# Kernel optimization log

Hardware: AMD Instinct MI355X
Metric: run time of the kernel (lower is better)

## Reference

```python
import jax, jax.numpy as jnp
import numpy as np

B, S, D = 4, 4096, 2048
SCAN, STATE = 128, 16


def setup_inputs() -> dict:
    key = jax.random.key(0)
    ks = jax.random.split(key, 8)
    scale = 1.0 / np.sqrt(D)
    scale_s = 1.0 / np.sqrt(SCAN)
    x = jax.random.normal(ks[0], (B, S, D), dtype=jnp.float32)
    Wi = jax.random.normal(ks[1], (SCAN, D), dtype=jnp.float32) * scale
    Wo = jax.random.normal(ks[2], (D, SCAN), dtype=jnp.float32) * 0.02  # torch zero-inits; small random for nontrivial output
    A_log = jax.random.normal(ks[3], (SCAN, STATE), dtype=jnp.float32) * 0.1
    Wb = jax.random.normal(ks[4], (STATE, SCAN), dtype=jnp.float32) * scale_s
    Wc = jax.random.normal(ks[5], (STATE, SCAN), dtype=jnp.float32) * scale_s
    Wdt = jax.random.normal(ks[6], (SCAN, SCAN), dtype=jnp.float32) * scale_s
    b_dt = jnp.full((SCAN,), -3.0, dtype=jnp.float32)
    Wg = jax.random.normal(ks[7], (SCAN, D), dtype=jnp.float32) * scale
    return {"x": x, "Wi": Wi, "Wo": Wo, "A_log": A_log, "Wb": Wb,
            "Wc": Wc, "Wdt": Wdt, "b_dt": b_dt, "Wg": Wg}


def _selective_scan_ffn(x, Wi, Wo, A_log, Wb, Wc, Wdt, b_dt, Wg):
    z = jnp.einsum('bsd,nd->bsn', x, Wi)                      # [B,S,SCAN]
    gate = jax.nn.silu(jnp.einsum('bsd,nd->bsn', x, Wg))      # [B,S,SCAN]
    A = -jnp.exp(A_log)                                        # [SCAN,STATE]
    B_in = jnp.einsum('bsn,kn->bsk', z, Wb)                   # [B,S,STATE]
    C_in = jnp.einsum('bsn,kn->bsk', z, Wc)                   # [B,S,STATE]
    dt = jax.nn.softplus(jnp.einsum('bsn,mn->bsm', z, Wdt) + b_dt)  # [B,S,SCAN]
    A_bar = 1.0 + dt[..., None] * A                            # [B,S,SCAN,STATE]

    def step(state, inp):
        a_t, dt_t, z_t, b_t, c_t = inp
        # state: [B,SCAN,STATE]
        state = a_t * state + dt_t[..., None] * (z_t[..., None] * b_t[:, None, :])
        y = jnp.einsum('bnk,bk->bn', state, c_t)               # [B,SCAN]
        return state, y

    xs = (jnp.moveaxis(A_bar, 1, 0), jnp.moveaxis(dt, 1, 0),
          jnp.moveaxis(z, 1, 0), jnp.moveaxis(B_in, 1, 0), jnp.moveaxis(C_in, 1, 0))
    state0 = jnp.zeros((x.shape[0], Wi.shape[0], A_log.shape[1]), dtype=x.dtype)
    _, ys = jax.lax.scan(step, state0, xs)                     # [S,B,SCAN]
    y = jnp.moveaxis(ys, 0, 1) * gate                          # [B,S,SCAN]
    return jnp.einsum('bsn,dn->bsd', y, Wo)                    # [B,S,D]


def reference(x, Wi, Wo, A_log, Wb, Wc, Wdt, b_dt, Wg):
    return _selective_scan_ffn(x, Wi, Wo, A_log, Wb, Wc, Wdt, b_dt, Wg)
```

## Files before the change

### kernel.cpp

```cpp
#include <hip/hip_runtime.h>
#include <hip/hip_bf16.h>
#include <math.h>

using bf16 = __hip_bfloat16;
typedef __attribute__((ext_vector_type(8))) short bf16x8;
typedef __attribute__((ext_vector_type(8))) short short8;
typedef __attribute__((ext_vector_type(4))) float f32x4;

#define AS1 __attribute__((address_space(1)))
#define AS3 __attribute__((address_space(3)))

constexpr int BATCH = 4;
constexpr int SEQ   = 4096;
constexpr int DIM   = 2048;
constexpr int SCAN  = 128;
constexpr int STATE = 16;
constexpr int LCH   = 16;
constexpr int NCH   = SEQ / LCH;

__device__ __forceinline__ float bf2f(bf16 v) { return __bfloat162float(v); }
__device__ __forceinline__ bf16  f2bf(float v) { return __float2bfloat16(v); }
__device__ __forceinline__ float bfbits(unsigned short u) {
  return __uint_as_float((unsigned)u << 16);
}

__device__ __forceinline__ int probe_dtype(const unsigned short* __restrict__ xp) {
  int cnt = 0;
#pragma unroll
  for (int i = 0; i < 64; ++i) {
    int e = (xp[i] >> 7) & 0xFF;
    cnt += (e >= 107 && e <= 147) ? 1 : 0;
  }
  return (cnt >= 51) ? 1 : 0;
}

__device__ __forceinline__ void conv_b(const void* src, bf16* dst, int n, int f,
                                       int gtid, int nt) {
  if (f) { const bf16* s = (const bf16*)src;  for (int i = gtid; i < n; i += nt) dst[i] = s[i]; }
  else   { const float* s = (const float*)src; for (int i = gtid; i < n; i += nt) dst[i] = f2bf(s[i]); }
}
__device__ __forceinline__ void conv_f(const void* src, float* dst, int n, int f,
                                       int gtid, int nt) {
  if (f) { const bf16* s = (const bf16*)src;  for (int i = gtid; i < n; i += nt) dst[i] = bf2f(s[i]); }
  else   { const float* s = (const float*)src; for (int i = gtid; i < n; i += nt) dst[i] = s[i]; }
}
__device__ __forceinline__ void conv_aneg(const void* src, float* dst, int n, int f,
                                          int gtid, int nt) {
  if (f) { const bf16* s = (const bf16*)src;  for (int i = gtid; i < n; i += nt) dst[i] = -expf(bf2f(s[i])); }
  else   { const float* s = (const float*)src; for (int i = gtid; i < n; i += nt) dst[i] = -expf(s[i]); }
}

__global__ __launch_bounds__(256) void kconv_w(
    const unsigned short* __restrict__ xprobe,
    const void* Wi, const void* Wg, const void* Wo, const void* Wdt,
    const void* Wb, const void* Wc, const void* bdt, const void* Alog,
    bf16* Wzg, bf16* Wob, bf16* Wdtb, bf16* Wbb, bf16* Wcb,
    float* bdtf, float* Anegf, int* __restrict__ flag) {
  int f = probe_dtype(xprobe);
  if (blockIdx.x == 0 && threadIdx.x == 0) *flag = f;
  int nt = gridDim.x * blockDim.x;
  int g  = blockIdx.x * blockDim.x + threadIdx.x;
  conv_b(Wi,  Wzg,               SCAN * DIM,  f, g, nt);
  conv_b(Wg,  Wzg + SCAN * DIM,  SCAN * DIM,  f, g, nt);
  conv_b(Wo,  Wob,  DIM * SCAN,  f, g, nt);
  conv_b(Wdt, Wdtb, SCAN * SCAN, f, g, nt);
  conv_b(Wb,  Wbb,  STATE * SCAN, f, g, nt);
  conv_b(Wc,  Wcb,  STATE * SCAN, f, g, nt);
  conv_f(bdt,  bdtf,  SCAN,          f, g, nt);
  conv_aneg(Alog, Anegf, SCAN * STATE, f, g, nt);
}

__device__ __forceinline__ int swzb(int row, int colbyte) {
  return row * 128 + (colbyte ^ ((row & 7) << 4));
}

struct ARegs { float4 v; };

template <int F>
__device__ __forceinline__ ARegs loadA(const void* __restrict__ xin, size_t rowbase,
                                       int k0, int ae) {
  ARegs r;
  if (F) {
    float2 t = *(const float2*)((const bf16*)xin + rowbase + k0 + ae);
    r.v.x = t.x; r.v.y = t.y; r.v.z = 0.f; r.v.w = 0.f;
  } else {
    r.v = *(const float4*)((const float*)xin + rowbase + k0 + ae);
  }
  return r;
}

template <int F>
__device__ __forceinline__ void writeA(char* abuf, int ar, int ae, const ARegs& rg) {
  char* d = abuf + swzb(ar, ae * 2);
  if (F) {
    *(float2*)d = make_float2(rg.v.x, rg.v.y);
  } else {
    union { float2 f2; bf16 b[4]; } u;
    u.b[0] = f2bf(rg.v.x); u.b[1] = f2bf(rg.v.y);
    u.b[2] = f2bf(rg.v.z); u.b[3] = f2bf(rg.v.w);
    *(float2*)d = u.f2;
  }
}

__device__ __forceinline__ void stageB(const bf16* __restrict__ W, int k0,
                                       char* bbuf, int tid) {
  int w = tid >> 6;
#pragma unroll
  for (int i = 0; i < 2; ++i) {
    int off = i * 16384 + tid * 16;
    int r   = off >> 7;
    int cbl = off & 127;
    int cbs = cbl ^ ((r & 7) << 4);
    const bf16* src = W + (size_t)r * DIM + k0 + (cbs >> 1);
    char* lb = bbuf + i * 16384 + w * 1024;
    __builtin_amdgcn_global_load_lds((const AS1 void*)src, (AS3 void*)lb, 16, 0, 0);
  }
}

__device__ __forceinline__ void compute64x256_16w(const char* abuf, const char* bbuf,
                                                  int tid, f32x4 acc[2][2]) {
  int l = tid & 63, w = tid >> 6;
  int wr = (w >> 3) * 32;
  int wc = (w & 7) * 32;
  int lr = l & 15, lk = (l >> 4) * 8;
#pragma unroll
  for (int kk = 0; kk < 64; kk += 32) {
    int cb = (kk + lk) * 2;
    bf16x8 a[2], b[2];
#pragma unroll
    for (int m = 0; m < 2; ++m)
      a[m] = *(const bf16x8*)(abuf + swzb(wr + m * 16 + lr, cb));
#pragma unroll
    for (int n = 0; n < 2; ++n)
      b[n] = *(const bf16x8*)(bbuf + swzb(wc + n * 16 + lr, cb));
#pragma unroll
    for (int m = 0; m < 2; ++m)
#pragma unroll
      for (int n = 0; n < 2; ++n)
        acc[m][n] = __builtin_amdgcn_mfma_f32_16x16x32_bf16(a[m], b[n], acc[m][n], 0, 0, 0);
  }
}

__device__ __forceinline__ void vm_wait3() { asm volatile("s_waitcnt vmcnt(3)" ::: "memory"); __builtin_amdgcn_sched_barrier(0); }
__device__ __forceinline__ void vm_wait0() { asm volatile("s_waitcnt vmcnt(0)" ::: "memory"); __builtin_amdgcn_sched_barrier(0); }
__device__ __forceinline__ void lgkm0_barrier() {
  asm volatile("s_waitcnt lgkmcnt(0)" ::: "memory");
  __builtin_amdgcn_sched_barrier(0);
  __builtin_amdgcn_s_barrier();
}

template <int F>
__device__ __forceinline__ void k1_main(const void* __restrict__ xin,
                                        const bf16* __restrict__ W,
                                        char* lds, size_t xrow, int ar, int ae,
                                        int tid, f32x4 acc[2][2]) {
  constexpr int NK = DIM / 64;
  constexpr int BUF = 40960;
  ARegs aH = loadA<F>(xin, xrow, 0, ae);
  stageB(W, 0, lds + 0 * BUF + 8192, tid);
  ARegs aN = loadA<F>(xin, xrow, 64, ae);
  stageB(W, 64, lds + 1 * BUF + 8192, tid);
  vm_wait3();
  writeA<F>(lds + 0 * BUF, ar, ae, aH);
  aH = aN;
  lgkm0_barrier();

  for (int t = 0; t < NK; ++t) {
    char* curb = lds + (t % 3) * BUF;
    if (t + 2 < NK) {
      aN = loadA<F>(xin, xrow, (t + 2) * 64, ae);
      stageB(W, (t + 2) * 64, lds + ((t + 2) % 3) * BUF + 8192, tid);
    }
    compute64x256_16w(curb, curb + 8192, tid, acc);
    if (t + 1 < NK) {
      if (t + 2 < NK) vm_wait3();
      else            vm_wait0();
      writeA<F>(lds + ((t + 1) % 3) * BUF, ar, ae, aH);
      aH = aN;
      lgkm0_barrier();
    }
  }
}

__global__ __launch_bounds__(1024) void k12_zg(const void* __restrict__ xin,
                                               const bf16* __restrict__ Wzg,
                                               const bf16* __restrict__ Wdtb,
                                               const bf16* __restrict__ Wbb,
                                               const bf16* __restrict__ Wcb,
                                               const float* __restrict__ bdtf,
                                               const float* __restrict__ Aneg,
                                               bf16* __restrict__ z,
                                               bf16* __restrict__ gate,
                                               float* __restrict__ dt,
                                               float* __restrict__ Bv,
                                               float* __restrict__ Cv,
                                               float* __restrict__ fin,
                                               float* __restrict__ apr,
                                               const int* __restrict__ flag) {
  __shared__ char lds[122880];
  int tid = threadIdx.x;
  int mb  = blockIdx.x;
  int m0  = mb * 64;
  int f   = *flag;
  int ar  = tid >> 4;
  int ae  = (tid & 15) * 4;
  size_t xrow = ((size_t)m0 + ar) * DIM;

  f32x4 acc[2][2];
#pragma unroll
  for (int m = 0; m < 2; ++m)
#pragma unroll
    for (int n = 0; n < 2; ++n)
#pragma unroll
      for (int j = 0; j < 4; ++j) acc[m][n][j] = 0.f;

  if (f) k1_main<1>(xin, Wzg, lds, xrow, ar, ae, tid, acc);
  else   k1_main<0>(xin, Wzg, lds, xrow, ar, ae, tid, acc);

  __syncthreads();

  bf16 (*zl)[128]   = (bf16 (*)[128])(lds);
  bf16 (*wl)[136]   = (bf16 (*)[136])(lds + 16384);
  bf16 (*dtlb)[128] = (bf16 (*)[128])(lds + 59904);
  bf16 (*Blcb)[16]  = (bf16 (*)[16]) (lds + 76288);

  {
    int l = tid & 63, w = tid >> 6;
    int wr = (w >> 3) * 32;
    int wcg = (w & 7) * 32;
    int sel = wcg >> 7;
    int cb  = wcg & 127;
    int lr = l & 15, lj = (l >> 4) * 4;
    bf16* o = sel ? gate : z;
#pragma unroll
    for (int m = 0; m < 2; ++m)
#pragma unroll
      for (int n = 0; n < 2; ++n)
#pragma unroll
        for (int j = 0; j < 4; ++j) {
          int rowl = wr + m * 16 + lj + j;
          int col  = cb + n * 16 + lr;
          float v = acc[m][n][j];
          if (sel) v = v / (1.f + expf(-v));
          bf16 bv = f2bf(v);
          o[(size_t)(m0 + rowl) * SCAN + col] = bv;
          if (!sel) zl[rowl][col] = bv;
        }
  }
  for (int idx = tid; idx < 160 * 16; idx += 1024) {
    int r = idx >> 4, c8 = (idx & 15) << 3;
    const bf16* src;
    if (r < 128)      src = Wdtb + r * 128;
    else if (r < 144) src = Wbb + (r - 128) * 128;
    else              src = Wcb + (r - 144) * 128;
    *(short8*)&wl[r][c8] = *(const short8*)(src + c8);
  }
  __syncthreads();

  if (tid < 256) {
    int l = tid & 63, w = tid >> 6;
    int lr = l & 15, lk = (l >> 4) * 8, lj = (l >> 4) * 4;
    f32x4 acc2[10];
#pragma unroll
    for (int n = 0; n < 10; ++n)
#pragma unroll
      for (int j = 0; j < 4; ++j) acc2[n][j] = 0.f;

#pragma unroll
    for (int kk = 0; kk < 128; kk += 32) {
      bf16x8 a = *(const bf16x8*)&zl[w * 16 + lr][kk + lk];
#pragma unroll
      for (int n = 0; n < 10; ++n) {
        bf16x8 bfr = *(const bf16x8*)&wl[n * 16 + lr][kk + lk];
        acc2[n] = __builtin_amdgcn_mfma_f32_16x16x32_bf16(a, bfr, acc2[n], 0, 0, 0);
      }
    }

#pragma unroll
    for (int n = 0; n < 10; ++n) {
      int o = n * 16 + lr;
#pragma unroll
      for (int j = 0; j < 4; ++j) {
        int row = w * 16 + lj + j;
        float v = acc2[n][j];
        if (o < 128) {
          v += bdtf[o];
          v = fmaxf(v, 0.f) + log1pf(expf(-fabsf(v)));
          dt[(size_t)(m0 + row) * SCAN + o] = v;
          dtlb[row][o] = f2bf(v);
        } else if (o < 144) {
          Bv[(size_t)(m0 + row) * STATE + (o - 128)] = v;
          Blcb[row][o - 128] = f2bf(v);
        } else {
          Cv[(size_t)(m0 + row) * STATE + (o - 144)] = v;
        }
      }
    }
  }
  __syncthreads();

  if (tid < 512) {
    int n  = tid & 127;
    int cc = tid >> 7;
    int b   = m0 >> 12;
    int ch0 = (m0 & 4095) >> 4;
    float A[STATE];
#pragma unroll
    for (int k = 0; k < STATE; ++k) A[k] = Aneg[n * STATE + k];

    float st[STATE], ap[STATE];
#pragma unroll
    for (int k = 0; k < STATE; ++k) { st[k] = 0.f; ap[k] = 1.f; }
#pragma unroll
    for (int t = 0; t < LCH; ++t) {
      int row = cc * LCH + t;
      float d = bf2f(dtlb[row][n]);
      float u = d * bf2f(zl[row][n]);
#pragma unroll
      for (int kg = 0; kg < 4; ++kg) {
        unsigned long long bb = *(const unsigned long long*)&Blcb[row][kg * 4];
        float b0 = bfbits((unsigned short)bb);
        float b1 = bfbits((unsigned short)(bb >> 16));
        float b2 = bfbits((unsigned short)(bb >> 32));
        float b3 = bfbits((unsigned short)(bb >> 48));
        float a;
        a = fmaf(d, A[kg*4+0], 1.f); st[kg*4+0] = fmaf(a, st[kg*4+0], u * b0); ap[kg*4+0] *= a;
        a = fmaf(d, A[kg*4+1], 1.f); st[kg*4+1] = fmaf(a, st[kg*4+1], u * b1); ap[kg*4+1] *= a;
        a = fmaf(d, A[kg*4+2], 1.f); st[kg*4+2] = fmaf(a, st[kg*4+2], u * b2); ap[kg*4+2] *= a;
        a = fmaf(d, A[kg*4+3], 1.f); st[kg*4+3] = fmaf(a, st[kg*4+3], u * b3); ap[kg*4+3] *= a;
      }
    }
    size_t base = ((size_t)b * NCH + (ch0 + cc)) * (STATE * SCAN) + n;
#pragma unroll
    for (int k = 0; k < STATE; ++k) {
      fin[base + k * SCAN] = st[k];
      apr[base + k * SCAN] = ap[k];
    }
  }
}

__global__ __launch_bounds__(64) void k3b(const float* __restrict__ fin,
                                          float* __restrict__ apr) {
  int c  = blockIdx.x * 64 + threadIdx.x;
  int b  = c >> 11;
  int kn = c & 2047;
  size_t base = (size_t)b * NCH * 2048 + kn;
  float s = 0.f;
  for (int g = 0; g < NCH; g += 16) {
    float fv[16], av[16];
#pragma unroll
    for (int i = 0; i < 16; ++i) {
      size_t o = base + (size_t)(g + i) * 2048;
      fv[i] = fin[o];
      av[i] = apr[o];
    }
#pragma unroll
    for (int i = 0; i < 16; ++i) {
      size_t o = base + (size_t)(g + i) * 2048;
      apr[o] = s;
      s = fmaf(av[i], s, fv[i]);
    }
  }
}

__global__ __launch_bounds__(128) void k3c(
    const float* __restrict__ dt, const bf16* z,
    const float* __restrict__ Bv, const float* __restrict__ Cv,
    const float* __restrict__ Aneg, const float* __restrict__ inc,
    const bf16* __restrict__ gate, bf16* yg) {
  __shared__ float Bl[LCH][STATE];
  __shared__ float Cl[LCH][STATE];
  int n  = threadIdx.x;
  int ch = blockIdx.x, b = blockIdx.y;
  int t0 = ch * LCH;
  if (n < LCH * STATE / 4)
    ((float4*)&Bl[0][0])[n] = ((const float4*)(Bv + ((size_t)b * SEQ + t0) * STATE))[n];
  else if (n < LCH * STATE / 2)
    ((float4*)&Cl[0][0])[n - LCH * STATE / 4] =
        ((const float4*)(Cv + ((size_t)b * SEQ + t0) * STATE))[n - LCH * STATE / 4];

  size_t base = ((size_t)b * NCH + ch) * (STATE * SCAN) + n;
  float A[STATE], st[STATE];
#pragma unroll
  for (int k = 0; k < STATE; ++k) {
    A[k]  = Aneg[n * STATE + k];
    st[k] = inc[base + k * SCAN];
  }
  __syncthreads();

  const float* dtp = dt   + ((size_t)b * SEQ + t0) * SCAN + n;
  const bf16*  zp  = z    + ((size_t)b * SEQ + t0) * SCAN + n;
  const bf16*  gp  = gate + ((size_t)b * SEQ + t0) * SCAN + n;
  bf16*        yp  = yg   + ((size_t)b * SEQ + t0) * SCAN + n;
#pragma unroll 4
  for (int t = 0; t < LCH; ++t) {
    float d = dtp[t * SCAN];
    float u = d * bf2f(zp[t * SCAN]);
    float g = bf2f(gp[t * SCAN]);
    float y0 = 0.f, y1 = 0.f, y2 = 0.f, y3 = 0.f;
#pragma unroll
    for (int kg = 0; kg < 4; ++kg) {
      float4 B4 = *(const float4*)&Bl[t][kg * 4];
      float4 C4 = *(const float4*)&Cl[t][kg * 4];
      float a, p = 0.f;
      a = fmaf(d, A[kg*4+0], 1.f); st[kg*4+0] = fmaf(a, st[kg*4+0], u * B4.x); p = fmaf(st[kg*4+0], C4.x, p);
      a = fmaf(d, A[kg*4+1], 1.f); st[kg*4+1] = fmaf(a, st[kg*4+1], u * B4.y); p = fmaf(st[kg*4+1], C4.y, p);
      a = fmaf(d, A[kg*4+2], 1.f); st[kg*4+2] = fmaf(a, st[kg*4+2], u * B4.z); p = fmaf(st[kg*4+2], C4.z, p);
      a = fmaf(d, A[kg*4+3], 1.f); st[kg*4+3] = fmaf(a, st[kg*4+3], u * B4.w); p = fmaf(st[kg*4+3], C4.w, p);
      if (kg == 0) y0 = p; else if (kg == 1) y1 = p; else if (kg == 2) y2 = p; else y3 = p;
    }
    float y = (y0 + y1) + (y2 + y3);
    yp[t * SCAN] = f2bf(y * g);
  }
}

__device__ __forceinline__ int swz256(int row, int colbyte) {
  return row * 256 + (colbyte ^ ((row & 7) << 4));
}

__global__ __launch_bounds__(256) void k4_out(const bf16* __restrict__ yg,
                                              const bf16* __restrict__ Wo,
                                              void* __restrict__ outv,
                                              const int* __restrict__ flag) {
  __shared__ char lds[49152];
  int tid = threadIdx.x;
  int mb = blockIdx.x, nb = blockIdx.y;
  int w = tid >> 6;

#pragma unroll
  for (int i = 0; i < 8; ++i) {
    int off = i * 4096 + tid * 16;
    int r   = off >> 8;
    int cbl = off & 255;
    int cbs = cbl ^ ((r & 7) << 4);
    const bf16* src = yg + (size_t)(mb * 128 + r) * SCAN + (cbs >> 1);
    __builtin_amdgcn_global_load_lds((const AS1 void*)src,
                                     (AS3 void*)(lds + i * 4096 + w * 1024), 16, 0, 0);
  }
#pragma unroll
  for (int i = 0; i < 4; ++i) {
    int off = i * 4096 + tid * 16;
    int r   = off >> 8;
    int cbl = off & 255;
    int cbs = cbl ^ ((r & 7) << 4);
    const bf16* src = Wo + (size_t)(nb * 64 + r) * SCAN + (cbs >> 1);
    __builtin_amdgcn_global_load_lds((const AS1 void*)src,
                                     (AS3 void*)(lds + 32768 + i * 4096 + w * 1024), 16, 0, 0);
  }
  __syncthreads();

  int l = tid & 63;
  int lr = l & 15, lk = (l >> 4) * 8;
  f32x4 acc[2][4];
#pragma unroll
  for (int m = 0; m < 2; ++m)
#pragma unroll
    for (int n = 0; n < 4; ++n)
#pragma unroll
      for (int j = 0; j < 4; ++j) acc[m][n][j] = 0.f;

#pragma unroll
  for (int kk = 0; kk < 128; kk += 32) {
    int cb = (kk + lk) * 2;
    bf16x8 a[2], b[4];
#pragma unroll
    for (int m = 0; m < 2; ++m)
      a[m] = *(const bf16x8*)(lds + swz256(w * 32 + m * 16 + lr, cb));
#pragma unroll
    for (int n = 0; n < 4; ++n)
      b[n] = *(const bf16x8*)(lds + 32768 + swz256(n * 16 + lr, cb));
#pragma unroll
    for (int m = 0; m < 2; ++m)
#pragma unroll
      for (int n = 0; n < 4; ++n)
        acc[m][n] = __builtin_amdgcn_mfma_f32_16x16x32_bf16(a[m], b[n], acc[m][n], 0, 0, 0);
  }

  int f = *flag;
  int lj = (l >> 4) * 4;
#pragma unroll
  for (int m = 0; m < 2; ++m)
#pragma unroll
    for (int n = 0; n < 4; ++n)
#pragma unroll
      for (int j = 0; j < 4; ++j) {
        int row = mb * 128 + w * 32 + m * 16 + lj + j;
        int col = nb * 64 + n * 16 + lr;
        size_t off = (size_t)row * DIM + col;
        float v = acc[m][n][j];
        if (f) ((bf16*)outv)[off] = f2bf(v);
        else   ((float*)outv)[off] = v;
      }
}

extern "C" void kernel_launch(void* const* d_in, const int* in_sizes, int n_in,
                              void* d_out, int out_size, void* d_ws, size_t ws_size,
                              hipStream_t stream) {
  const void* x     = d_in[0];
  const void* Wi    = d_in[1];
  const void* Wo    = d_in[2];
  const void* A_log = d_in[3];
  const void* Wb    = d_in[4];
  const void* Wc    = d_in[5];
  const void* Wdt   = d_in[6];
  const void* b_dt  = d_in[7];
  const void* Wg    = d_in[8];

  const size_t M = (size_t)BATCH * SEQ;
  char* p = (char*)d_ws;
  int*   flag = (int*)p;    p += 256;
  bf16*  Wzg  = (bf16*)p;   p += (size_t)2 * SCAN * DIM * 2;
  bf16*  Wob  = (bf16*)p;   p += (size_t)DIM * SCAN * 2;
  bf16*  Wdtb = (bf16*)p;   p += (size_t)SCAN * SCAN * 2;
  bf16*  Wbb  = (bf16*)p;   p += (size_t)STATE * SCAN * 2;
  bf16*  Wcb  = (bf16*)p;   p += (size_t)STATE * SCAN * 2;
  float* bdtf = (float*)p;  p += SCAN * 4;
  float* Anegf= (float*)p;  p += (size_t)SCAN * STATE * 4;
  bf16*  z    = (bf16*)p;   p += M * SCAN * 2;
  bf16*  gate = (bf16*)p;   p += M * SCAN * 2;
  bf16*  yg   = z;
  float* dt   = (float*)p;  p += M * SCAN * 4;
  float* Bv   = (float*)p;  p += M * STATE * 4;
  float* Cv   = (float*)p;  p += M * STATE * 4;
  float* fin  = (float*)p;  p += (size_t)BATCH * NCH * SCAN * STATE * 4;
  float* apr  = (float*)p;  p += (size_t)BATCH * NCH * SCAN * STATE * 4;

  kconv_w <<<256, 256, 0, stream>>>((const unsigned short*)x,
                                    Wi, Wg, Wo, Wdt, Wb, Wc, b_dt, A_log,
                                    Wzg, Wob, Wdtb, Wbb, Wcb, bdtf, Anegf, flag);
  k12_zg  <<<dim3(256), 1024, 0, stream>>>(x, Wzg, Wdtb, Wbb, Wcb, bdtf, Anegf,
                                           z, gate, dt, Bv, Cv, fin, apr, flag);
  k3b     <<<dim3(128), 64, 0, stream>>>(fin, apr);
  k3c     <<<dim3(NCH, BATCH), 128, 0, stream>>>(dt, z, Bv, Cv, Anegf, apr, gate, yg);
  k4_out  <<<dim3(128, 32), 256, 0, stream>>>(yg, Wob, d_out, flag);
}
```

Measured before the change: 131.1 us.

## Fuse chunk scan with output projection GEMM via LDS-staged activations

Merges the chunked scan kernel and the output projection GEMM into one kernel. Gated scan outputs for a 64-row tile are written to swizzled LDS and consumed directly by MFMA against Wo loaded from global memory. This removes the intermediate yg global write/read and one kernel launch. In exchange, the scan is recomputed for each of the two column halves, and register pressure rises with larger accumulator tiles.

```diff
diff --git a/kernel.cpp b/kernel.cpp
--- a/kernel.cpp
+++ b/kernel.cpp
@@ -363,134 +363,116 @@
   }
 }
 
-__global__ __launch_bounds__(128) void k3c(
-    const float* __restrict__ dt, const bf16* z,
+__device__ __forceinline__ int swz256(int row, int colbyte) {
+  return row * 256 + (colbyte ^ ((row & 7) << 4));
+}
+
+__global__ __launch_bounds__(512) void k34(
+    const float* __restrict__ dt, const bf16* __restrict__ z,
     const float* __restrict__ Bv, const float* __restrict__ Cv,
     const float* __restrict__ Aneg, const float* __restrict__ inc,
-    const bf16* __restrict__ gate, bf16* yg) {
-  __shared__ float Bl[LCH][STATE];
-  __shared__ float Cl[LCH][STATE];
-  int n  = threadIdx.x;
-  int ch = blockIdx.x, b = blockIdx.y;
-  int t0 = ch * LCH;
-  if (n < LCH * STATE / 4)
-    ((float4*)&Bl[0][0])[n] = ((const float4*)(Bv + ((size_t)b * SEQ + t0) * STATE))[n];
-  else if (n < LCH * STATE / 2)
-    ((float4*)&Cl[0][0])[n - LCH * STATE / 4] =
-        ((const float4*)(Cv + ((size_t)b * SEQ + t0) * STATE))[n - LCH * STATE / 4];
-
-  size_t base = ((size_t)b * NCH + ch) * (STATE * SCAN) + n;
-  float A[STATE], st[STATE];
-#pragma unroll
-  for (int k = 0; k < STATE; ++k) {
-    A[k]  = Aneg[n * STATE + k];
-    st[k] = inc[base + k * SCAN];
+    const bf16* __restrict__ gate, const bf16* __restrict__ Wob,
+    void* __restrict__ outv, const int* __restrict__ flag) {
+  __shared__ char lds[25088];
+  char*  ygl = lds;
+  float (*Bl)[STATE] = (float (*)[STATE])(lds + 16384);
+  float (*Cl)[STATE] = (float (*)[STATE])(lds + 20480);
+  int tid = threadIdx.x;
+  int mb  = blockIdx.x;
+  int nb  = blockIdx.y;
+  int m0  = mb * 64;
+
+  if (tid < 256)      ((float4*)&Bl[0][0])[tid]       = ((const float4*)(Bv + (size_t)m0 * STATE))[tid];
+  else                ((float4*)&Cl[0][0])[tid - 256] = ((const float4*)(Cv + (size_t)m0 * STATE))[tid - 256];
+
+  {
+    int n  = tid & 127;
+    int cc = tid >> 7;
+    int b   = m0 >> 12;
+    int ch0 = (m0 & 4095) >> 4;
+    size_t base = ((size_t)b * NCH + (ch0 + cc)) * (STATE * SCAN) + n;
+    float A[STATE], st[STATE];
+#pragma unroll
+    for (int k = 0; k < STATE; ++k) {
+      A[k]  = Aneg[n * STATE + k];
+      st[k] = inc[base + k * SCAN];
+    }
+    __syncthreads();
+
+    const float* dtp = dt   + ((size_t)m0 + cc * LCH) * SCAN + n;
+    const bf16*  zp  = z    + ((size_t)m0 + cc * LCH) * SCAN + n;
+    const bf16*  gp  = gate + ((size_t)m0 + cc * LCH) * SCAN + n;
+#pragma unroll
+    for (int t = 0; t < LCH; ++t) {
+      int row = cc * LCH + t;
+      float d = dtp[t * SCAN];
+      float u = d * bf2f(zp[t * SCAN]);
+      float g = bf2f(gp[t * SCAN]);
+      float y0 = 0.f, y1 = 0.f, y2 = 0.f, y3 = 0.f;
+#pragma unroll
+      for (int kg = 0; kg < 4; ++kg) {
+        float4 B4 = *(const float4*)&Bl[row][kg * 4];
+        float4 C4 = *(const float4*)&Cl[row][kg * 4];
+        float a, p = 0.f;
+        a = fmaf(d, A[kg*4+0], 1.f); st[kg*4+0] = fmaf(a, st[kg*4+0], u * B4.x); p = fmaf(st[kg*4+0], C4.x, p);
+        a = fmaf(d, A[kg*4+1], 1.f); st[kg*4+1] = fmaf(a, st[kg*4+1], u * B4.y); p = fmaf(st[kg*4+1], C4.y, p);
+        a = fmaf(d, A[kg*4+2], 1.f); st[kg*4+2] = fmaf(a, st[kg*4+2], u * B4.z); p = fmaf(st[kg*4+2], C4.z, p);
+        a = fmaf(d, A[kg*4+3], 1.f); st[kg*4+3] = fmaf(a, st[kg*4+3], u * B4.w); p = fmaf(st[kg*4+3], C4.w, p);
+        if (kg == 0) y0 = p; else if (kg == 1) y1 = p; else if (kg == 2) y2 = p; else y3 = p;
+      }
+      float y = (y0 + y1) + (y2 + y3);
+      *(bf16*)(ygl + swz256(row, n * 2)) = f2bf(y * g);
+    }
   }
   __syncthreads();
 
-  const float* dtp = dt   + ((size_t)b * SEQ + t0) * SCAN + n;
-  const bf16*  zp  = z    + ((size_t)b * SEQ + t0) * SCAN + n;
-  const bf16*  gp  = gate + ((size_t)b * SEQ + t0) * SCAN + n;
-  bf16*        yp  = yg   + ((size_t)b * SEQ + t0) * SCAN + n;
-#pragma unroll 4
-  for (int t = 0; t < LCH; ++t) {
-    float d = dtp[t * SCAN];
-    float u = d * bf2f(zp[t * SCAN]);
-    float g = bf2f(gp[t * SCAN]);
-    float y0 = 0.f, y1 = 0.f, y2 = 0.f, y3 = 0.f;
-#pragma unroll
-    for (int kg = 0; kg < 4; ++kg) {
-      float4 B4 = *(const float4*)&Bl[t][kg * 4];
-      float4 C4 = *(const float4*)&Cl[t][kg * 4];
-      float a, p = 0.f;
-      a = fmaf(d, A[kg*4+0], 1.f); st[kg*4+0] = fmaf(a, st[kg*4+0], u * B4.x); p = fmaf(st[kg*4+0], C4.x, p);
-      a = fmaf(d, A[kg*4+1], 1.f); st[kg*4+1] = fmaf(a, st[kg*4+1], u * B4.y); p = fmaf(st[kg*4+1], C4.y, p);
-      a = fmaf(d, A[kg*4+2], 1.f); st[kg*4+2] = fmaf(a, st[kg*4+2], u * B4.z); p = fmaf(st[kg*4+2], C4.z, p);
-      a = fmaf(d, A[kg*4+3], 1.f); st[kg*4+3] = fmaf(a, st[kg*4+3], u * B4.w); p = fmaf(st[kg*4+3], C4.w, p);
-      if (kg == 0) y0 = p; else if (kg == 1) y1 = p; else if (kg == 2) y2 = p; else y3 = p;
-    }
-    float y = (y0 + y1) + (y2 + y3);
-    yp[t * SCAN] = f2bf(y * g);
-  }
-}
-
-__device__ __forceinline__ int swz256(int row, int colbyte) {
-  return row * 256 + (colbyte ^ ((row & 7) << 4));
-}
-
-__global__ __launch_bounds__(256) void k4_out(const bf16* __restrict__ yg,
-                                              const bf16* __restrict__ Wo,
-                                              void* __restrict__ outv,
-                                              const int* __restrict__ flag) {
-  __shared__ char lds[49152];
-  int tid = threadIdx.x;
-  int mb = blockIdx.x, nb = blockIdx.y;
-  int w = tid >> 6;
-
-#pragma unroll
-  for (int i = 0; i < 8; ++i) {
-    int off = i * 4096 + tid * 16;
-    int r   = off >> 8;
-    int cbl = off & 255;
-    int cbs = cbl ^ ((r & 7) << 4);
-    const bf16* src = yg + (size_t)(mb * 128 + r) * SCAN + (cbs >> 1);
-    __builtin_amdgcn_global_load_lds((const AS1 void*)src,
-                                     (AS3 void*)(lds + i * 4096 + w * 1024), 16, 0, 0);
-  }
-#pragma unroll
-  for (int i = 0; i < 4; ++i) {
-    int off = i * 4096 + tid * 16;
-    int r   = off >> 8;
-    int cbl = off & 255;
-    int cbs = cbl ^ ((r & 7) << 4);
-    const bf16* src = Wo + (size_t)(nb * 64 + r) * SCAN + (cbs >> 1);
-    __builtin_amdgcn_global_load_lds((const AS1 void*)src,
-                                     (AS3 void*)(lds + 32768 + i * 4096 + w * 1024), 16, 0, 0);
-  }
-  __syncthreads();
-
-  int l = tid & 63;
+  int l = tid & 63, w = tid >> 6;
   int lr = l & 15, lk = (l >> 4) * 8;
-  f32x4 acc[2][4];
-#pragma unroll
-  for (int m = 0; m < 2; ++m)
-#pragma unroll
-    for (int n = 0; n < 4; ++n)
-#pragma unroll
-      for (int j = 0; j < 4; ++j) acc[m][n][j] = 0.f;
-
-#pragma unroll
-  for (int kk = 0; kk < 128; kk += 32) {
-    int cb = (kk + lk) * 2;
-    bf16x8 a[2], b[4];
-#pragma unroll
-    for (int m = 0; m < 2; ++m)
-      a[m] = *(const bf16x8*)(lds + swz256(w * 32 + m * 16 + lr, cb));
-#pragma unroll
-    for (int n = 0; n < 4; ++n)
-      b[n] = *(const bf16x8*)(lds + 32768 + swz256(n * 16 + lr, cb));
-#pragma unroll
-    for (int m = 0; m < 2; ++m)
+  int f = *flag;
+  int colw = nb * 1024 + w * 128;
+#pragma unroll
+  for (int g2 = 0; g2 < 2; ++g2) {
+    int nc0 = colw + g2 * 64;
+    f32x4 acc[4][4];
+#pragma unroll
+    for (int m = 0; m < 4; ++m)
 #pragma unroll
       for (int n = 0; n < 4; ++n)
-        acc[m][n] = __builtin_amdgcn_mfma_f32_16x16x32_bf16(a[m], b[n], acc[m][n], 0, 0, 0);
-  }
-
-  int f = *flag;
-  int lj = (l >> 4) * 4;
-#pragma unroll
-  for (int m = 0; m < 2; ++m)
-#pragma unroll
-    for (int n = 0; n < 4; ++n)
-#pragma unroll
-      for (int j = 0; j < 4; ++j) {
-        int row = mb * 128 + w * 32 + m * 16 + lj + j;
-        int col = nb * 64 + n * 16 + lr;
-        size_t off = (size_t)row * DIM + col;
-        float v = acc[m][n][j];
-        if (f) ((bf16*)outv)[off] = f2bf(v);
-        else   ((float*)outv)[off] = v;
-      }
+#pragma unroll
+        for (int j = 0; j < 4; ++j) acc[m][n][j] = 0.f;
+
+#pragma unroll
+    for (int kk = 0; kk < 128; kk += 32) {
+      int cb = (kk + lk) * 2;
+      bf16x8 a[4], b[4];
+#pragma unroll
+      for (int m = 0; m < 4; ++m)
+        a[m] = *(const bf16x8*)(ygl + swz256(m * 16 + lr, cb));
+#pragma unroll
+      for (int n = 0; n < 4; ++n)
+        b[n] = *(const bf16x8*)(Wob + (size_t)(nc0 + n * 16 + lr) * SCAN + kk + lk);
+#pragma unroll
+      for (int m = 0; m < 4; ++m)
+#pragma unroll
+        for (int n = 0; n < 4; ++n)
+          acc[m][n] = __builtin_amdgcn_mfma_f32_16x16x32_bf16(a[m], b[n], acc[m][n], 0, 0, 0);
+    }
+
+    int lj = (l >> 4) * 4;
+#pragma unroll
+    for (int m = 0; m < 4; ++m)
+#pragma unroll
+      for (int n = 0; n < 4; ++n)
+#pragma unroll
+        for (int j = 0; j < 4; ++j) {
+          int row = m0 + m * 16 + lj + j;
+          int col = nc0 + n * 16 + lr;
+          size_t off = (size_t)row * DIM + col;
+          float v = acc[m][n][j];
+          if (f) ((bf16*)outv)[off] = f2bf(v);
+          else   ((float*)outv)[off] = v;
+        }
+  }
 }
 
 extern "C" void kernel_launch(void* const* d_in, const int* in_sizes, int n_in,
@@ -518,7 +500,6 @@
   float* Anegf= (float*)p;  p += (size_t)SCAN * STATE * 4;
   bf16*  z    = (bf16*)p;   p += M * SCAN * 2;
   bf16*  gate = (bf16*)p;   p += M * SCAN * 2;
-  bf16*  yg   = z;
   float* dt   = (float*)p;  p += M * SCAN * 4;
   float* Bv   = (float*)p;  p += M * STATE * 4;
   float* Cv   = (float*)p;  p += M * STATE * 4;
@@ -531,6 +512,6 @@
   k12_zg  <<<dim3(256), 1024, 0, stream>>>(x, Wzg, Wdtb, Wbb, Wcb, bdtf, Anegf,
                                            z, gate, dt, Bv, Cv, fin, apr, flag);
   k3b     <<<dim3(128), 64, 0, stream>>>(fin, apr);
-  k3c     <<<dim3(NCH, BATCH), 128, 0, stream>>>(dt, z, Bv, Cv, Anegf, apr, gate, yg);
-  k4_out  <<<dim3(128, 32), 256, 0, stream>>>(yg, Wob, d_out, flag);
-}
+  k34     <<<dim3(256, 2), 512, 0, stream>>>(dt, z, Bv, Cv, Anegf, apr, gate,
+                                             Wob, d_out, flag);
+}
```

Result: no change. 133.7 us (+2.0%).
